# Optimization experiments

Hardware: AMD Instinct MI355X
Metric: run time of the kernel (lower is better)

## Reference

```python
import jax, jax.numpy as jnp
import numpy as np

N_TRAIN = 131072
M_TEST = 65536
T_SPAN = 100.0
D = 3  # Matern-5/2 state dim


def setup_inputs() -> dict:
    key = jax.random.key(0)
    k1, k2, k3, k4 = jax.random.split(key, 4)
    times = jnp.sort(jax.random.uniform(k1, (N_TRAIN,), jnp.float32) * T_SPAN)
    t_star = jnp.sort(jax.random.uniform(k2, (M_TEST,), jnp.float32) * T_SPAN)
    # positive site precisions, site naturals scaled so pseudo-targets are O(1)
    site_nat2 = jax.random.uniform(k3, (N_TRAIN,), jnp.float32) * 4.0 + 0.5
    site_nat1 = jax.random.normal(k4, (N_TRAIN,), jnp.float32) * site_nat2
    return dict(
        times=times,
        t_star=t_star,
        site_nat1=site_nat1,
        site_nat2=site_nat2,
        variance=jnp.float32(1.0),
        lengthscale=jnp.float32(0.5),
        mean_const=jnp.float32(0.1),
    )


def _matern52_sde(variance, lengthscale):
    lam = jnp.sqrt(5.0).astype(jnp.float32) / lengthscale
    F = jnp.array([[0.0, 1.0, 0.0],
                   [0.0, 0.0, 1.0],
                   [0.0, 0.0, 0.0]], jnp.float32)
    F = F.at[2, 0].set(-lam ** 3).at[2, 1].set(-3.0 * lam ** 2).at[2, 2].set(-3.0 * lam)
    kappa = lam ** 2 / 3.0
    P_inf = variance * jnp.array([[1.0, 0.0, 0.0],
                                  [0.0, 0.0, 0.0],
                                  [0.0, 0.0, 0.0]], jnp.float32)
    P_inf = P_inf.at[0, 2].set(-variance * kappa)
    P_inf = P_inf.at[2, 0].set(-variance * kappa)
    P_inf = P_inf.at[1, 1].set(variance * kappa)
    P_inf = P_inf.at[2, 2].set(variance * lam ** 4)
    H = jnp.array([[1.0, 0.0, 0.0]], jnp.float32)
    return F, H, P_inf, lam


def _discretise(F, P_inf, lam, dt):
    # (F + lam I) is nilpotent of index 3 -> exact expm
    I = jnp.eye(D, dtype=jnp.float32)
    Nm = F + lam * I
    Nm2 = Nm @ Nm
    dt_ = dt[:, None, None]
    A = jnp.exp(-lam * dt)[:, None, None] * (I + dt_ * Nm + 0.5 * dt_ ** 2 * Nm2)
    APA = jnp.einsum('tij,jk,tlk->til', A, P_inf, A)
    Q = P_inf - APA
    return A, Q


def _kalman_filter(H, P_inf, A_seq, Q_seq, residual, is_obs, R_full):
    h = H[0]  # [D]

    def step(carry, inp):
        m, P = carry
        A, Q, r, obs, R = inp
        m_pred = A @ m
        P_pred = A @ P @ A.T + Q
        S = h @ P_pred @ h + R
        K = obs * (P_pred @ h) / S  # masked gain: test points skip update
        v = r - m_pred @ h
        m_f = m_pred + K * v
        P_f = P_pred - jnp.outer(K, K) * S
        return (m_f, P_f), (m_pred, P_pred, m_f, P_f)

    init = (jnp.zeros(D, jnp.float32), P_inf)
    _, (m_pred, P_pred, m_filt, P_filt) = jax.lax.scan(
        step, init, (A_seq, Q_seq, residual, is_obs, R_full))
    return m_pred, P_pred, m_filt, P_filt


def _rts_smoother(m_pred, P_pred, m_filt, P_filt, A_seq):
    def back(carry, inp):
        m_s_next, P_s_next = carry
        m_f, P_f, A_n, m_p_n, P_p_n = inp
        G = jnp.linalg.solve(P_p_n, A_n @ P_f).T  # P_f A^T P_pred^{-1}
        m_s = m_f + G @ (m_s_next - m_p_n)
        P_s = P_f + G @ (P_s_next - P_p_n) @ G.T
        return (m_s, P_s), (m_s, P_s)

    init = (m_filt[-1], P_filt[-1])
    xs = (m_filt[:-1], P_filt[:-1], A_seq[1:], m_pred[1:], P_pred[1:])
    _, (m_s, P_s) = jax.lax.scan(back, init, xs, reverse=True)
    m_smooth = jnp.concatenate([m_s, m_filt[-1:]], axis=0)
    P_smooth = jnp.concatenate([P_s, P_filt[-1:]], axis=0)
    return m_smooth, P_smooth


def reference(times, t_star, site_nat1, site_nat2, variance, lengthscale, mean_const):
    F, H, P_inf, lam = _matern52_sde(variance, lengthscale)
    N = times.shape[0]
    M = t_star.shape[0]
    merged = jnp.concatenate([times, t_star])
    order = jnp.argsort(merged)  # jnp.argsort is stable
    merged_sorted = merged[order]
    is_obs = jnp.concatenate([jnp.ones(N, jnp.float32), jnp.zeros(M, jnp.float32)])[order]
    pseudo_targets = site_nat1 / site_nat2
    residual_full = jnp.concatenate([pseudo_targets - mean_const,
                                     jnp.zeros(M, jnp.float32)])[order]
    R_full = jnp.concatenate([jnp.reciprocal(site_nat2), jnp.ones(M, jnp.float32)])[order]
    dt_full = jnp.concatenate([jnp.zeros(1, jnp.float32), jnp.diff(merged_sorted)])
    A_seq, Q_seq = _discretise(F, P_inf, lam, dt_full)
    m_pred, P_pred, m_filt, P_filt = _kalman_filter(
        H, P_inf, A_seq, Q_seq, residual_full, is_obs, R_full)
    m_smooth, P_smooth = _rts_smoother(m_pred, P_pred, m_filt, P_filt, A_seq)
    inv_order = jnp.argsort(order)
    test_positions = inv_order[N:]
    m_test = m_smooth[test_positions]
    P_test = P_smooth[test_positions]
    means = m_test @ H[0] + mean_const  # H = [1,0,0]
    vars_ = jnp.einsum('i,tij,j->t', H[0], P_test, H[0])
    return means, jnp.maximum(vars_, 0.0)
```

## Files before the change

### kernel.cpp

```cpp
#include <hip/hip_runtime.h>
#include <math.h>

#define DEV __device__ __forceinline__

constexpr int N_TRAIN = 131072;
constexpr int M_TEST  = 65536;
constexpr int T_TOT   = N_TRAIN + M_TEST;
constexpr int TPB     = 64;
constexpr int NBLK    = T_TOT / TPB;
constexpr int GRP     = 64;
constexpr int NGRP    = NBLK / GRP;
constexpr int FE_S    = 33;
constexpr int SE_S    = 19;

DEV void mm(const float* X, const float* Y, float* Z) {
#pragma unroll
  for (int i = 0; i < 3; ++i)
#pragma unroll
    for (int j = 0; j < 3; ++j)
      Z[i*3+j] = X[i*3]*Y[j] + X[i*3+1]*Y[3+j] + X[i*3+2]*Y[6+j];
}
DEV void mmnt(const float* X, const float* Y, float* Z) {
#pragma unroll
  for (int i = 0; i < 3; ++i)
#pragma unroll
    for (int j = 0; j < 3; ++j)
      Z[i*3+j] = X[i*3]*Y[j*3] + X[i*3+1]*Y[j*3+1] + X[i*3+2]*Y[j*3+2];
}
DEV void mtn(const float* X, const float* Y, float* Z) {
#pragma unroll
  for (int i = 0; i < 3; ++i)
#pragma unroll
    for (int j = 0; j < 3; ++j)
      Z[i*3+j] = X[i]*Y[j] + X[3+i]*Y[3+j] + X[6+i]*Y[6+j];
}
DEV void mv(const float* X, const float* v, float* w) {
#pragma unroll
  for (int i = 0; i < 3; ++i) w[i] = X[i*3]*v[0] + X[i*3+1]*v[1] + X[i*3+2]*v[2];
}
DEV void mtv(const float* X, const float* v, float* w) {
#pragma unroll
  for (int i = 0; i < 3; ++i) w[i] = X[i]*v[0] + X[3+i]*v[1] + X[6+i]*v[2];
}
DEV void inv3(const float* mf_, float* o) {
  double m0=mf_[0], m1=mf_[1], m2=mf_[2], m3=mf_[3], m4=mf_[4],
         m5=mf_[5], m6=mf_[6], m7=mf_[7], m8=mf_[8];
  double c00 = m4*m8 - m5*m7;
  double c10 = m5*m6 - m3*m8;
  double c20 = m3*m7 - m4*m6;
  double det = m0*c00 + m1*c10 + m2*c20;
  double id = 1.0 / det;
  o[0] = (float)(c00*id); o[1] = (float)((m2*m7-m1*m8)*id); o[2] = (float)((m1*m5-m2*m4)*id);
  o[3] = (float)(c10*id); o[4] = (float)((m0*m8-m2*m6)*id); o[5] = (float)((m2*m3-m0*m5)*id);
  o[6] = (float)(c20*id); o[7] = (float)((m1*m6-m0*m7)*id); o[8] = (float)((m0*m4-m1*m3)*id);
}
DEV void symm(float* P) {
  float a = 0.5f*(P[1]+P[3]), b = 0.5f*(P[2]+P[6]), c = 0.5f*(P[5]+P[7]);
  P[1]=P[3]=a; P[2]=P[6]=b; P[5]=P[7]=c;
}

struct Model { float lam, v, kap, l4; };
DEV Model make_model(const float* varp, const float* ellp) {
  Model M; M.v = varp[0];
  float ell = ellp[0];
  M.lam = sqrtf(5.0f) / ell;
  M.kap = M.lam * M.lam / 3.0f;
  float l2 = M.lam * M.lam;
  M.l4 = l2 * l2;
  return M;
}
DEV void pinf(const Model& M, float* P) {
  float vk = M.v * M.kap;
  P[0]=M.v; P[1]=0;  P[2]=-vk;
  P[3]=0;   P[4]=vk; P[5]=0;
  P[6]=-vk; P[7]=0;  P[8]=M.v*M.l4;
}
DEV void make_AQ(const Model& M, float dt, float* A, float* Q) {
  float lam = M.lam, l2 = lam*lam, l3 = l2*lam, l4 = M.l4;
  float e = __expf(-lam * dt);
  float h = 0.5f * dt * dt;
  A[0] = e*(1.0f + dt*lam + h*l2);
  A[1] = e*(dt + 2.0f*h*lam);
  A[2] = e*h;
  A[3] = e*(-h*l3);
  A[4] = e*(1.0f + dt*lam - 2.0f*h*l2);
  A[5] = e*(dt - h*lam);
  A[6] = e*(-dt*l3 + h*l4);
  A[7] = e*(-3.0f*dt*l2 + 2.0f*h*l3);
  A[8] = e*(1.0f - 2.0f*dt*lam + h*l2);
  float vk = M.v * M.kap, vl4 = M.v * M.l4;
  float B[9];
#pragma unroll
  for (int i = 0; i < 3; ++i) {
    B[i*3+0] =  A[i*3+0]*M.v - A[i*3+2]*vk;
    B[i*3+1] =  A[i*3+1]*vk;
    B[i*3+2] = -A[i*3+0]*vk  + A[i*3+2]*vl4;
  }
  float Pi[9]; pinf(M, Pi);
#pragma unroll
  for (int i = 0; i < 3; ++i)
#pragma unroll
    for (int j = 0; j < 3; ++j)
      Q[i*3+j] = Pi[i*3+j] - (B[i*3]*A[j*3] + B[i*3+1]*A[j*3+1] + B[i*3+2]*A[j*3+2]);
}

struct FE { float A[9]; float b[3]; float C[9]; float h[3]; float J[9]; };

DEV FE fe_identity() {
  FE e;
#pragma unroll
  for (int i=0;i<9;++i){ e.A[i]=0.0f; e.C[i]=0.0f; e.J[i]=0.0f; }
  e.A[0]=e.A[4]=e.A[8]=1.0f;
  e.b[0]=e.b[1]=e.b[2]=0.0f; e.h[0]=e.h[1]=e.h[2]=0.0f;
  return e;
}
DEV void fe_store(const FE& e, float* g) {
#pragma unroll
  for (int i=0;i<9;++i) g[i]=e.A[i];
  g[9]=e.b[0]; g[10]=e.b[1]; g[11]=e.b[2];
#pragma unroll
  for (int i=0;i<9;++i) g[12+i]=e.C[i];
  g[21]=e.h[0]; g[22]=e.h[1]; g[23]=e.h[2];
#pragma unroll
  for (int i=0;i<9;++i) g[24+i]=e.J[i];
}
DEV FE fe_load(const float* g) {
  FE e;
#pragma unroll
  for (int i=0;i<9;++i) e.A[i]=g[i];
  e.b[0]=g[9]; e.b[1]=g[10]; e.b[2]=g[11];
#pragma unroll
  for (int i=0;i<9;++i) e.C[i]=g[12+i];
  e.h[0]=g[21]; e.h[1]=g[22]; e.h[2]=g[23];
#pragma unroll
  for (int i=0;i<9;++i) e.J[i]=g[24+i];
  return e;
}
DEV void fe_storeT(const FE& e, float* g, int idx, int n) {
#pragma unroll
  for (int i=0;i<9;++i) g[i*n+idx]=e.A[i];
#pragma unroll
  for (int i=0;i<3;++i) g[(9+i)*n+idx]=e.b[i];
#pragma unroll
  for (int i=0;i<9;++i) g[(12+i)*n+idx]=e.C[i];
#pragma unroll
  for (int i=0;i<3;++i) g[(21+i)*n+idx]=e.h[i];
#pragma unroll
  for (int i=0;i<9;++i) g[(24+i)*n+idx]=e.J[i];
}
DEV FE fe_loadT(const float* g, int idx, int n) {
  FE e;
#pragma unroll
  for (int i=0;i<9;++i) e.A[i]=g[i*n+idx];
#pragma unroll
  for (int i=0;i<3;++i) e.b[i]=g[(9+i)*n+idx];
#pragma unroll
  for (int i=0;i<9;++i) e.C[i]=g[(12+i)*n+idx];
#pragma unroll
  for (int i=0;i<3;++i) e.h[i]=g[(21+i)*n+idx];
#pragma unroll
  for (int i=0;i<9;++i) e.J[i]=g[(24+i)*n+idx];
  return e;
}
DEV FE build_felem(const Model& M, float dt, float obsf, float rf, float Rf_, bool first) {
  FE E;
  float r = rf, R = Rf_;
  float g = (obsf > 0.5f) ? 1.0f : 0.0f;
  if (first) {
#pragma unroll
    for (int i=0;i<9;++i){ E.A[i]=0.0f; E.J[i]=0.0f; }
    E.h[0]=E.h[1]=E.h[2]=0.0f;
    float Pi[9]; pinf(M, Pi);
    float S = Pi[0] + R;
    float f = g / S;
    float K0=Pi[0]*f, K1=Pi[3]*f, K2=Pi[6]*f;
    E.b[0]=K0*r; E.b[1]=K1*r; E.b[2]=K2*r;
    E.C[0]=Pi[0]-S*K0*K0; E.C[1]=Pi[1]-S*K0*K1; E.C[2]=Pi[2]-S*K0*K2;
    E.C[3]=Pi[3]-S*K1*K0; E.C[4]=Pi[4]-S*K1*K1; E.C[5]=Pi[5]-S*K1*K2;
    E.C[6]=Pi[6]-S*K2*K0; E.C[7]=Pi[7]-S*K2*K1; E.C[8]=Pi[8]-S*K2*K2;
    return E;
  }
  float Am[9], Q[9]; make_AQ(M, dt, Am, Q);
  float S = Q[0] + R, iS = g / S;
  float K0=Q[0]*iS, K1=Q[3]*iS, K2=Q[6]*iS;
#pragma unroll
  for (int j = 0; j < 3; ++j) {
    E.A[j]   = Am[j]   - K0*Am[j];
    E.A[3+j] = Am[3+j] - K1*Am[j];
    E.A[6+j] = Am[6+j] - K2*Am[j];
    E.C[j]   = Q[j]    - K0*Q[j];
    E.C[3+j] = Q[3+j]  - K1*Q[j];
    E.C[6+j] = Q[6+j]  - K2*Q[j];
  }
  E.b[0]=K0*r; E.b[1]=K1*r; E.b[2]=K2*r;
  float riS = r*iS;
  E.h[0]=Am[0]*riS; E.h[1]=Am[1]*riS; E.h[2]=Am[2]*riS;
#pragma unroll
  for (int i = 0; i < 3; ++i)
#pragma unroll
    for (int j = 0; j < 3; ++j)
      E.J[i*3+j] = Am[i]*Am[j]*iS;
  return E;
}
DEV FE fcompose(const FE& x, const FE& y) {
  const float *A1=x.A,*b1=x.b,*C1=x.C,*h1=x.h,*J1=x.J;
  const float *A2=y.A,*b2=y.b,*C2=y.C,*h2=y.h,*J2=y.J;
  FE o;
  float Mx[9]; mm(C1,J2,Mx); Mx[0]+=1.0f; Mx[4]+=1.0f; Mx[8]+=1.0f;
  float Mi[9]; inv3(Mx,Mi);
  float T1[9]; mm(A2,Mi,T1);
  mm(T1,A1,o.A);
  float u[3]; mv(C1,h2,u); u[0]+=b1[0]; u[1]+=b1[1]; u[2]+=b1[2];
  mv(T1,u,o.b); o.b[0]+=b2[0]; o.b[1]+=b2[1]; o.b[2]+=b2[2];
  float t2[9]; mm(T1,C1,t2);
  mmnt(t2,A2,o.C);
#pragma unroll
  for (int i=0;i<9;++i) o.C[i]+=C2[i];
  float tmp[9]; mm(Mi,A1,tmp);
  float w[3]; mv(J2,b1,w);
  w[0]=h2[0]-w[0]; w[1]=h2[1]-w[1]; w[2]=h2[2]-w[2];
  mtv(tmp,w,o.h); o.h[0]+=h1[0]; o.h[1]+=h1[1]; o.h[2]+=h1[2];
  float V[9]; mm(J2,A1,V);
  mtn(tmp,V,o.J);
#pragma unroll
  for (int i=0;i<9;++i) o.J[i]+=J1[i];
  symm(o.C); symm(o.J);
  return o;
}
DEV void fstep(const Model& M, float dt, float obsf, float rf, float Rf_,
               float* m, float* P) {
  float A[9], Q[9]; make_AQ(M, dt, A, Q);
  float mp[3]; mv(A, m, mp);
  float W[9]; mmnt(P, A, W);
  float Pp[9]; mm(A, W, Pp);
#pragma unroll
  for (int i=0;i<9;++i) Pp[i]+=Q[i];
  float S = Pp[0] + Rf_;
  float f = (obsf > 0.5f) ? (1.0f/S) : 0.0f;
  float K0=Pp[0]*f, K1=Pp[3]*f, K2=Pp[6]*f;
  float v = rf - mp[0];
  m[0]=mp[0]+K0*v; m[1]=mp[1]+K1*v; m[2]=mp[2]+K2*v;
  P[0]=Pp[0]-S*K0*K0; P[1]=Pp[1]-S*K0*K1; P[2]=Pp[2]-S*K0*K2;
  P[3]=Pp[3]-S*K1*K0; P[4]=Pp[4]-S*K1*K1; P[5]=Pp[5]-S*K1*K2;
  P[6]=Pp[6]-S*K2*K0; P[7]=Pp[7]-S*K2*K1; P[8]=Pp[8]-S*K2*K2;
  symm(P);
}

struct SE { float G[9]; float c[3]; float U[9]; };

DEV SE se_identity() {
  SE s;
#pragma unroll
  for (int i=0;i<9;++i){ s.G[i]=0.0f; s.U[i]=0.0f; }
  s.G[0]=s.G[4]=s.G[8]=1.0f;
  s.c[0]=s.c[1]=s.c[2]=0.0f;
  return s;
}
DEV void se_store(const SE& s, float* g) {
#pragma unroll
  for (int i=0;i<9;++i) g[i]=s.G[i];
  g[9]=s.c[0]; g[10]=s.c[1]; g[11]=s.c[2];
  g[12]=s.U[0]; g[13]=s.U[1]; g[14]=s.U[2]; g[15]=s.U[4]; g[16]=s.U[5]; g[17]=s.U[8];
}
DEV SE se_load(const float* g) {
  SE s;
#pragma unroll
  for (int i=0;i<9;++i) s.G[i]=g[i];
  s.c[0]=g[9]; s.c[1]=g[10]; s.c[2]=g[11];
  s.U[0]=g[12]; s.U[1]=g[13]; s.U[2]=g[14];
  s.U[3]=g[13]; s.U[4]=g[15]; s.U[5]=g[16];
  s.U[6]=g[14]; s.U[7]=g[16]; s.U[8]=g[17];
  return s;
}
DEV void se_storeT(const SE& s, float* g, int idx, int n) {
#pragma unroll
  for (int i=0;i<9;++i) g[i*n+idx]=s.G[i];
#pragma unroll
  for (int i=0;i<3;++i) g[(9+i)*n+idx]=s.c[i];
  g[12*n+idx]=s.U[0]; g[13*n+idx]=s.U[1]; g[14*n+idx]=s.U[2];
  g[15*n+idx]=s.U[4]; g[16*n+idx]=s.U[5]; g[17*n+idx]=s.U[8];
}
DEV SE se_loadT(const float* g, int idx, int n) {
  SE s;
#pragma unroll
  for (int i=0;i<9;++i) s.G[i]=g[i*n+idx];
#pragma unroll
  for (int i=0;i<3;++i) s.c[i]=g[(9+i)*n+idx];
  float u0=g[12*n+idx], u1=g[13*n+idx], u2=g[14*n+idx],
        u4=g[15*n+idx], u5=g[16*n+idx], u8=g[17*n+idx];
  s.U[0]=u0; s.U[1]=u1; s.U[2]=u2;
  s.U[3]=u1; s.U[4]=u4; s.U[5]=u5;
  s.U[6]=u2; s.U[7]=u5; s.U[8]=u8;
  return s;
}
DEV SE scompose(const SE& x, const SE& y) {
  SE o;
  mm(x.G, y.G, o.G);
  float t[3]; mv(x.G, y.c, t);
  o.c[0]=t[0]+x.c[0]; o.c[1]=t[1]+x.c[1]; o.c[2]=t[2]+x.c[2];
  float T[9]; mm(x.G, y.U, T);
  mmnt(T, x.G, o.U);
#pragma unroll
  for (int i=0;i<9;++i) o.U[i]+=x.U[i];
  symm(o.U);
  return o;
}
DEV void sapply(const SE& s, float* m, float* P) {
  float t[3]; mv(s.G, m, t);
  float T[9]; mm(s.G, P, T);
  float Pn[9]; mmnt(T, s.G, Pn);
  m[0]=t[0]+s.c[0]; m[1]=t[1]+s.c[1]; m[2]=t[2]+s.c[2];
#pragma unroll
  for (int i=0;i<9;++i) P[i]=Pn[i]+s.U[i];
  symm(P);
}
DEV SE build_selem(const Model& M, const float4* pk, const float* mf, const float* Pf, int k) {
  float m[3] = { mf[k], mf[T_TOT+k], mf[2*T_TOT+k] };
  float p00=Pf[k], p01=Pf[T_TOT+k], p02=Pf[2*T_TOT+k],
        p11=Pf[3*T_TOT+k], p12=Pf[4*T_TOT+k], p22=Pf[5*T_TOT+k];
  float P[9] = { p00,p01,p02, p01,p11,p12, p02,p12,p22 };
  float dt = pk[k+1].x - pk[k].x;
  SE s;
  float A[9], Q[9]; make_AQ(M, dt, A, Q);
  float W[9]; mmnt(P, A, W);
  float Pp[9]; mm(A, W, Pp);
#pragma unroll
  for (int j=0;j<9;++j) Pp[j]+=Q[j];
  float Pi_[9]; inv3(Pp, Pi_);
  mm(W, Pi_, s.G);
  float mp[3]; mv(A, m, mp);
  float gm[3]; mv(s.G, mp, gm);
  s.c[0]=m[0]-gm[0]; s.c[1]=m[1]-gm[1]; s.c[2]=m[2]-gm[2];
  float GW[9]; mmnt(s.G, W, GW);
#pragma unroll
  for (int j=0;j<9;++j) s.U[j]=P[j]-GW[j];
  symm(s.U);
  return s;
}

__global__ void k_merge(const float* __restrict__ times, const float* __restrict__ tstar,
                        const float* __restrict__ n1, const float* __restrict__ n2,
                        const float* __restrict__ mcp,
                        float4* pk, int* oix) {
  int g = blockIdx.x*blockDim.x + threadIdx.x;
  if (g >= T_TOT) return;
  float mc = mcp[0];
  if (g < N_TRAIN) {
    int i = g;
    float t = times[i];
    int lo = 0, hi = M_TEST;
    while (lo < hi) { int mid=(lo+hi)>>1; if (tstar[mid] < t) lo=mid+1; else hi=mid; }
    int p = i + lo;
    float s2 = n2[i];
    pk[p] = make_float4(t, n1[i]/s2 - mc, 1.0f/s2, 1.0f);
    oix[p] = -1;
  } else {
    int j = g - N_TRAIN;
    float t = tstar[j];
    int lo = 0, hi = N_TRAIN;
    while (lo < hi) { int mid=(lo+hi)>>1; if (times[mid] <= t) lo=mid+1; else hi=mid; }
    int p = j + lo;
    pk[p] = make_float4(t, 0.f, 1.f, 0.f);
    oix[p] = j;
  }
}

__global__ __launch_bounds__(TPB, 2) void k_f1(
    const float* varp, const float* ellp, const float4* __restrict__ pk,
    float* tIncl, float* blkAgg) {
  __shared__ float lds[TPB*FE_S];
  int l = threadIdx.x, b = blockIdx.x;
  int t = b*TPB + l;
  Model M = make_model(varp, ellp);
  float4 q = pk[t];
  float dt = (t == 0) ? 0.0f : (q.x - pk[t-1].x);
  FE run = build_felem(M, dt, q.w, q.y, q.z, t == 0);
  fe_store(run, &lds[l*FE_S]);
  for (int d = 1; d < TPB; d <<= 1) {
    __syncthreads();
    FE oth; bool act = (l >= d);
    if (act) oth = fe_load(&lds[(l-d)*FE_S]);
    __syncthreads();
    if (act) { run = fcompose(oth, run); fe_store(run, &lds[l*FE_S]); }
  }
  fe_storeT(run, tIncl, t, T_TOT);
  if (l == TPB-1) fe_storeT(run, blkAgg, b, NBLK);
}

__global__ __launch_bounds__(TPB, 2) void k_f2a(const float* __restrict__ blkAgg,
                                                float* blkIncl2, float* grpAgg) {
  __shared__ float lds[TPB*FE_S];
  int l = threadIdx.x, gb = blockIdx.x;
  int b = gb*GRP + l;
  FE run = fe_loadT(blkAgg, b, NBLK);
  fe_store(run, &lds[l*FE_S]);
  for (int d = 1; d < TPB; d <<= 1) {
    __syncthreads();
    FE oth; bool act = (l >= d);
    if (act) oth = fe_load(&lds[(l-d)*FE_S]);
    __syncthreads();
    if (act) { run = fcompose(oth, run); fe_store(run, &lds[l*FE_S]); }
  }
  fe_storeT(run, blkIncl2, b, NBLK);
  if (l == GRP-1) fe_store(run, grpAgg + gb*FE_S);
}

__global__ __launch_bounds__(TPB, 2) void k_f2b(const float* __restrict__ grpAgg,
                                                float* grpPref) {
  __shared__ float lds[TPB*FE_S];
  int j = threadIdx.x;
  FE run = (j < NGRP) ? fe_load(grpAgg + j*FE_S) : fe_identity();
  fe_store(run, &lds[j*FE_S]);
  for (int d = 1; d < TPB; d <<= 1) {
    __syncthreads();
    FE oth; bool act = (j >= d);
    if (act) oth = fe_load(&lds[(j-d)*FE_S]);
    __syncthreads();
    if (act) { run = fcompose(oth, run); fe_store(run, &lds[j*FE_S]); }
  }
  __syncthreads();
  if (j < NGRP) {
    FE X = (j == 0) ? fe_identity() : fe_load(&lds[(j-1)*FE_S]);
    fe_store(X, grpPref + j*FE_S);
  }
}

__global__ __launch_bounds__(TPB, 2) void k_f3(
    const float* varp, const float* ellp, const float4* __restrict__ pk,
    const float* __restrict__ tIncl, const float* __restrict__ blkIncl2,
    const float* __restrict__ grpPref,
    float* mf, float* Pf, float* xT) {
  int l = threadIdx.x, b = blockIdx.x;
  int t = b*TPB + l;
  int g = b >> 6, lb = b & (GRP-1);
  Model M = make_model(varp, ellp);
  float m[3], P[9];
  if (t == 0) {
    m[0]=m[1]=m[2]=0.0f; pinf(M, P);
  } else {
    FE gp = fe_load(grpPref + g*FE_S);
    FE entB = (lb == 0) ? gp : fcompose(gp, fe_loadT(blkIncl2, b-1, NBLK));
    FE ent  = (l == 0) ? entB : fcompose(entB, fe_loadT(tIncl, t-1, T_TOT));
    m[0]=ent.b[0]; m[1]=ent.b[1]; m[2]=ent.b[2];
#pragma unroll
    for (int i=0;i<9;++i) P[i]=ent.C[i];
  }
  float4 q = pk[t];
  float dt = (t == 0) ? 0.0f : (q.x - pk[t-1].x);
  fstep(M, dt, q.w, q.y, q.z, m, P);
  mf[t]=m[0]; mf[T_TOT+t]=m[1]; mf[2*T_TOT+t]=m[2];
  Pf[t]=P[0]; Pf[T_TOT+t]=P[1]; Pf[2*T_TOT+t]=P[2];
  Pf[3*T_TOT+t]=P[4]; Pf[4*T_TOT+t]=P[5]; Pf[5*T_TOT+t]=P[8];
  if (t == T_TOT-1) {
    xT[0]=m[0]; xT[1]=m[1]; xT[2]=m[2];
    xT[3]=P[0]; xT[4]=P[1]; xT[5]=P[2];
    xT[6]=P[4]; xT[7]=P[5]; xT[8]=P[8];
  }
}

__global__ __launch_bounds__(TPB, 2) void k_s1(
    const float* varp, const float* ellp, const float4* __restrict__ pk,
    const float* __restrict__ mf, const float* __restrict__ Pf,
    float* tSuf, float* blkAggS) {
  __shared__ float lds[TPB*SE_S];
  int l = threadIdx.x, b = blockIdx.x;
  int t = b*TPB + l;
  Model M = make_model(varp, ellp);
  SE Macc = (t <= T_TOT-2) ? build_selem(M, pk, mf, Pf, t) : se_identity();
  se_store(Macc, &lds[l*SE_S]);
  for (int d = 1; d < TPB; d <<= 1) {
    __syncthreads();
    SE oth; bool act = (l + d < TPB);
    if (act) oth = se_load(&lds[(l+d)*SE_S]);
    __syncthreads();
    if (act) { Macc = scompose(Macc, oth); se_store(Macc, &lds[l*SE_S]); }
  }
  se_storeT(Macc, tSuf, t, T_TOT);
  if (l == 0) se_storeT(Macc, blkAggS, b, NBLK);
}

__global__ __launch_bounds__(TPB, 2) void k_s2a(const float* __restrict__ blkAggS,
                                                float* blkSuf2, float* grpAggS) {
  __shared__ float lds[TPB*SE_S];
  int l = threadIdx.x, gb = blockIdx.x;
  int b = gb*GRP + l;
  SE run = se_loadT(blkAggS, b, NBLK);
  se_store(run, &lds[l*SE_S]);
  for (int d = 1; d < TPB; d <<= 1) {
    __syncthreads();
    SE oth; bool act = (l + d < TPB);
    if (act) oth = se_load(&lds[(l+d)*SE_S]);
    __syncthreads();
    if (act) { run = scompose(run, oth); se_store(run, &lds[l*SE_S]); }
  }
  se_storeT(run, blkSuf2, b, NBLK);
  if (l == 0) se_store(run, grpAggS + gb*18);
}

__global__ __launch_bounds__(TPB, 2) void k_s2b(const float* __restrict__ grpAggS,
                                                const float* __restrict__ xT,
                                                float* gExit) {
  __shared__ float lds[TPB*SE_S];
  int j = threadIdx.x;
  SE run = (j < NGRP) ? se_load(grpAggS + j*18) : se_identity();
  se_store(run, &lds[j*SE_S]);
  for (int d = 1; d < TPB; d <<= 1) {
    __syncthreads();
    SE oth; bool act = (j + d < TPB);
    if (act) oth = se_load(&lds[(j+d)*SE_S]);
    __syncthreads();
    if (act) { run = scompose(run, oth); se_store(run, &lds[j*SE_S]); }
  }
  __syncthreads();
  if (j < NGRP) {
    float m[3] = { xT[0], xT[1], xT[2] };
    float P[9] = { xT[3],xT[4],xT[5], xT[4],xT[6],xT[7], xT[5],xT[7],xT[8] };
    if (j < NGRP-1) {
      SE Sx = se_load(&lds[(j+1)*SE_S]);
      sapply(Sx, m, P);
    }
    float* o = gExit + j*9;
    o[0]=m[0];o[1]=m[1];o[2]=m[2];o[3]=P[0];o[4]=P[1];o[5]=P[2];o[6]=P[4];o[7]=P[5];o[8]=P[8];
  }
}

__global__ __launch_bounds__(TPB, 2) void k_s3(
    const float* varp, const float* ellp, const float* mcp,
    const float4* __restrict__ pk,
    const float* __restrict__ mf, const float* __restrict__ Pf,
    const float* __restrict__ tSuf, const float* __restrict__ blkSuf2,
    const float* __restrict__ gExit,
    const int* __restrict__ oix, float* out) {
  int l = threadIdx.x, b = blockIdx.x;
  int t = b*TPB + l;
  int g = b >> 6, lb = b & (GRP-1);
  Model M = make_model(varp, ellp);
  float mc = mcp[0];
  const float* ge = gExit + g*9;
  float m[3] = { ge[0], ge[1], ge[2] };
  float P[9] = { ge[3],ge[4],ge[5], ge[4],ge[6],ge[7], ge[5],ge[7],ge[8] };
  if (lb < GRP-1) {
    SE s = se_loadT(blkSuf2, b+1, NBLK);
    sapply(s, m, P);
  }
  if (l < TPB-1) {
    SE s = se_loadT(tSuf, t+1, T_TOT);
    sapply(s, m, P);
  }
  if (t <= T_TOT-2) {
    SE e = build_selem(M, pk, mf, Pf, t);
    sapply(e, m, P);
  }
  int j = oix[t];
  if (j >= 0) { out[j] = m[0] + mc; out[M_TEST + j] = fmaxf(P[0], 0.0f); }
}

extern "C" void kernel_launch(void* const* d_in, const int* in_sizes, int n_in,
                              void* d_out, int out_size, void* d_ws, size_t ws_size,
                              hipStream_t stream) {
  const float* times = (const float*)d_in[0];
  const float* tstar = (const float*)d_in[1];
  const float* n1    = (const float*)d_in[2];
  const float* n2    = (const float*)d_in[3];
  const float* varp  = (const float*)d_in[4];
  const float* ellp  = (const float*)d_in[5];
  const float* mcp   = (const float*)d_in[6];
  float* out = (float*)d_out;

  size_t off = 0;
  auto take = [&](size_t bytes) {
    char* p = (char*)d_ws + off;
    off += (bytes + 255) & ~(size_t)255;
    return (void*)p;
  };
  float4* pk     = (float4*)take(sizeof(float4) * T_TOT);
  int*    oix    = (int*)   take(sizeof(int)    * T_TOT);
  float*  mf     = (float*) take(sizeof(float)  * 3 * T_TOT);
  float*  Pf     = (float*) take(sizeof(float)  * 6 * T_TOT);
  float*  tIncl  = (float*) take(sizeof(float)  * FE_S * T_TOT);
  float*  blkAgg = (float*) take(sizeof(float)  * FE_S * NBLK);
  float*  blkIncl2=(float*) take(sizeof(float)  * FE_S * NBLK);
  float*  grpAgg = (float*) take(sizeof(float)  * FE_S * NGRP);
  float*  grpPref= (float*) take(sizeof(float)  * FE_S * NGRP);
  float*  tSuf   = (float*) take(sizeof(float)  * 18 * T_TOT);
  float*  blkAggS= (float*) take(sizeof(float)  * 18 * NBLK);
  float*  blkSuf2= (float*) take(sizeof(float)  * 18 * NBLK);
  float*  grpAggS= (float*) take(sizeof(float)  * 18 * NGRP);
  float*  gExit  = (float*) take(sizeof(float)  * 9  * NGRP);
  float*  xT     = (float*) take(sizeof(float)  * 9);
  (void)ws_size; (void)in_sizes; (void)n_in; (void)out_size;

  k_merge<<<(T_TOT+255)/256, 256, 0, stream>>>(times, tstar, n1, n2, mcp, pk, oix);
  k_f1   <<<NBLK, TPB, 0, stream>>>(varp, ellp, pk, tIncl, blkAgg);
  k_f2a  <<<NGRP, TPB, 0, stream>>>(blkAgg, blkIncl2, grpAgg);
  k_f2b  <<<1, TPB, 0, stream>>>(grpAgg, grpPref);
  k_f3   <<<NBLK, TPB, 0, stream>>>(varp, ellp, pk, tIncl, blkIncl2, grpPref, mf, Pf, xT);
  k_s1   <<<NBLK, TPB, 0, stream>>>(varp, ellp, pk, mf, Pf, tSuf, blkAggS);
  k_s2a  <<<NGRP, TPB, 0, stream>>>(blkAggS, blkSuf2, grpAggS);
  k_s2b  <<<1, TPB, 0, stream>>>(grpAggS, xT, gExit);
  k_s3   <<<NBLK, TPB, 0, stream>>>(varp, ellp, mcp, pk, mf, Pf, tSuf, blkSuf2, gExit, oix, out);
}
```

Before: 157.1 us.

## Replace LDS scans with wavefront shuffles and cache smoother elements

Each 64-thread block is a single wavefront, so the Hillis-Steele scans in all six scan kernels now exchange elements with __shfl_up/__shfl_down instead of going through shared memory with two barriers per step. k_s1 also stores each smoother element to a new eSel buffer, so k_s3 loads it rather than rebuilding it from pk/mf/Pf. Some launch bounds are raised to allow more resident blocks. The trade-off is extra global traffic for eSel and compose work now done by every lane, including inactive ones; the identity element for the last smoother step must match the earlier skip.

```diff
diff --git a/kernel.cpp b/kernel.cpp
--- a/kernel.cpp
+++ b/kernel.cpp
@@ -11,7 +11,6 @@
 constexpr int GRP     = 64;
 constexpr int NGRP    = NBLK / GRP;
 constexpr int FE_S    = 33;
-constexpr int SE_S    = 19;
 
 DEV void mm(const float* X, const float* Y, float* Z) {
 #pragma unroll
@@ -162,6 +161,20 @@
   for (int i=0;i<9;++i) e.J[i]=g[(24+i)*n+idx];
   return e;
 }
+DEV FE fe_shfl_up(const FE& e, int d) {
+  FE o;
+#pragma unroll
+  for (int i=0;i<9;++i) o.A[i]=__shfl_up(e.A[i], d, 64);
+#pragma unroll
+  for (int i=0;i<3;++i) o.b[i]=__shfl_up(e.b[i], d, 64);
+#pragma unroll
+  for (int i=0;i<9;++i) o.C[i]=__shfl_up(e.C[i], d, 64);
+#pragma unroll
+  for (int i=0;i<3;++i) o.h[i]=__shfl_up(e.h[i], d, 64);
+#pragma unroll
+  for (int i=0;i<9;++i) o.J[i]=__shfl_up(e.J[i], d, 64);
+  return o;
+}
 DEV FE build_felem(const Model& M, float dt, float obsf, float rf, float Rf_, bool first) {
   FE E;
   float r = rf, R = Rf_;
@@ -292,6 +305,16 @@
   s.U[3]=u1; s.U[4]=u4; s.U[5]=u5;
   s.U[6]=u2; s.U[7]=u5; s.U[8]=u8;
   return s;
+}
+DEV SE se_shfl_down(const SE& s, int d) {
+  SE o;
+#pragma unroll
+  for (int i=0;i<9;++i) o.G[i]=__shfl_down(s.G[i], d, 64);
+#pragma unroll
+  for (int i=0;i<3;++i) o.c[i]=__shfl_down(s.c[i], d, 64);
+#pragma unroll
+  for (int i=0;i<9;++i) o.U[i]=__shfl_down(s.U[i], d, 64);
+  return o;
 }
 DEV SE scompose(const SE& x, const SE& y) {
   SE o;
@@ -365,23 +388,19 @@
   }
 }
 
-__global__ __launch_bounds__(TPB, 2) void k_f1(
+__global__ __launch_bounds__(TPB, 3) void k_f1(
     const float* varp, const float* ellp, const float4* __restrict__ pk,
     float* tIncl, float* blkAgg) {
-  __shared__ float lds[TPB*FE_S];
   int l = threadIdx.x, b = blockIdx.x;
   int t = b*TPB + l;
   Model M = make_model(varp, ellp);
   float4 q = pk[t];
   float dt = (t == 0) ? 0.0f : (q.x - pk[t-1].x);
   FE run = build_felem(M, dt, q.w, q.y, q.z, t == 0);
-  fe_store(run, &lds[l*FE_S]);
   for (int d = 1; d < TPB; d <<= 1) {
-    __syncthreads();
-    FE oth; bool act = (l >= d);
-    if (act) oth = fe_load(&lds[(l-d)*FE_S]);
-    __syncthreads();
-    if (act) { run = fcompose(oth, run); fe_store(run, &lds[l*FE_S]); }
+    FE oth = fe_shfl_up(run, d);
+    FE comp = fcompose(oth, run);
+    if (l >= d) run = comp;
   }
   fe_storeT(run, tIncl, t, T_TOT);
   if (l == TPB-1) fe_storeT(run, blkAgg, b, NBLK);
@@ -389,17 +408,13 @@
 
 __global__ __launch_bounds__(TPB, 2) void k_f2a(const float* __restrict__ blkAgg,
                                                 float* blkIncl2, float* grpAgg) {
-  __shared__ float lds[TPB*FE_S];
   int l = threadIdx.x, gb = blockIdx.x;
   int b = gb*GRP + l;
   FE run = fe_loadT(blkAgg, b, NBLK);
-  fe_store(run, &lds[l*FE_S]);
   for (int d = 1; d < TPB; d <<= 1) {
-    __syncthreads();
-    FE oth; bool act = (l >= d);
-    if (act) oth = fe_load(&lds[(l-d)*FE_S]);
-    __syncthreads();
-    if (act) { run = fcompose(oth, run); fe_store(run, &lds[l*FE_S]); }
+    FE oth = fe_shfl_up(run, d);
+    FE comp = fcompose(oth, run);
+    if (l >= d) run = comp;
   }
   fe_storeT(run, blkIncl2, b, NBLK);
   if (l == GRP-1) fe_store(run, grpAgg + gb*FE_S);
@@ -407,25 +422,21 @@
 
 __global__ __launch_bounds__(TPB, 2) void k_f2b(const float* __restrict__ grpAgg,
                                                 float* grpPref) {
-  __shared__ float lds[TPB*FE_S];
   int j = threadIdx.x;
   FE run = (j < NGRP) ? fe_load(grpAgg + j*FE_S) : fe_identity();
-  fe_store(run, &lds[j*FE_S]);
   for (int d = 1; d < TPB; d <<= 1) {
-    __syncthreads();
-    FE oth; bool act = (j >= d);
-    if (act) oth = fe_load(&lds[(j-d)*FE_S]);
-    __syncthreads();
-    if (act) { run = fcompose(oth, run); fe_store(run, &lds[j*FE_S]); }
-  }
-  __syncthreads();
+    FE oth = fe_shfl_up(run, d);
+    FE comp = fcompose(oth, run);
+    if (j >= d) run = comp;
+  }
+  FE X = fe_shfl_up(run, 1);
   if (j < NGRP) {
-    FE X = (j == 0) ? fe_identity() : fe_load(&lds[(j-1)*FE_S]);
+    if (j == 0) X = fe_identity();
     fe_store(X, grpPref + j*FE_S);
   }
 }
 
-__global__ __launch_bounds__(TPB, 2) void k_f3(
+__global__ __launch_bounds__(TPB, 3) void k_f3(
     const float* varp, const float* ellp, const float4* __restrict__ pk,
     const float* __restrict__ tIncl, const float* __restrict__ blkIncl2,
     const float* __restrict__ grpPref,
@@ -458,22 +469,20 @@
   }
 }
 
-__global__ __launch_bounds__(TPB, 2) void k_s1(
+__global__ __launch_bounds__(TPB, 3) void k_s1(
     const float* varp, const float* ellp, const float4* __restrict__ pk,
     const float* __restrict__ mf, const float* __restrict__ Pf,
-    float* tSuf, float* blkAggS) {
-  __shared__ float lds[TPB*SE_S];
+    float* eSel, float* tSuf, float* blkAggS) {
   int l = threadIdx.x, b = blockIdx.x;
   int t = b*TPB + l;
   Model M = make_model(varp, ellp);
-  SE Macc = (t <= T_TOT-2) ? build_selem(M, pk, mf, Pf, t) : se_identity();
-  se_store(Macc, &lds[l*SE_S]);
+  SE e = (t <= T_TOT-2) ? build_selem(M, pk, mf, Pf, t) : se_identity();
+  se_storeT(e, eSel, t, T_TOT);
+  SE Macc = e;
   for (int d = 1; d < TPB; d <<= 1) {
-    __syncthreads();
-    SE oth; bool act = (l + d < TPB);
-    if (act) oth = se_load(&lds[(l+d)*SE_S]);
-    __syncthreads();
-    if (act) { Macc = scompose(Macc, oth); se_store(Macc, &lds[l*SE_S]); }
+    SE oth = se_shfl_down(Macc, d);
+    SE comp = scompose(Macc, oth);
+    if (l + d < TPB) Macc = comp;
   }
   se_storeT(Macc, tSuf, t, T_TOT);
   if (l == 0) se_storeT(Macc, blkAggS, b, NBLK);
@@ -481,17 +490,13 @@
 
 __global__ __launch_bounds__(TPB, 2) void k_s2a(const float* __restrict__ blkAggS,
                                                 float* blkSuf2, float* grpAggS) {
-  __shared__ float lds[TPB*SE_S];
   int l = threadIdx.x, gb = blockIdx.x;
   int b = gb*GRP + l;
   SE run = se_loadT(blkAggS, b, NBLK);
-  se_store(run, &lds[l*SE_S]);
   for (int d = 1; d < TPB; d <<= 1) {
-    __syncthreads();
-    SE oth; bool act = (l + d < TPB);
-    if (act) oth = se_load(&lds[(l+d)*SE_S]);
-    __syncthreads();
-    if (act) { run = scompose(run, oth); se_store(run, &lds[l*SE_S]); }
+    SE oth = se_shfl_down(run, d);
+    SE comp = scompose(run, oth);
+    if (l + d < TPB) run = comp;
   }
   se_storeT(run, blkSuf2, b, NBLK);
   if (l == 0) se_store(run, grpAggS + gb*18);
@@ -500,41 +505,31 @@
 __global__ __launch_bounds__(TPB, 2) void k_s2b(const float* __restrict__ grpAggS,
                                                 const float* __restrict__ xT,
                                                 float* gExit) {
-  __shared__ float lds[TPB*SE_S];
   int j = threadIdx.x;
   SE run = (j < NGRP) ? se_load(grpAggS + j*18) : se_identity();
-  se_store(run, &lds[j*SE_S]);
   for (int d = 1; d < TPB; d <<= 1) {
-    __syncthreads();
-    SE oth; bool act = (j + d < TPB);
-    if (act) oth = se_load(&lds[(j+d)*SE_S]);
-    __syncthreads();
-    if (act) { run = scompose(run, oth); se_store(run, &lds[j*SE_S]); }
-  }
-  __syncthreads();
+    SE oth = se_shfl_down(run, d);
+    SE comp = scompose(run, oth);
+    if (j + d < TPB) run = comp;
+  }
+  SE Sx = se_shfl_down(run, 1);
   if (j < NGRP) {
     float m[3] = { xT[0], xT[1], xT[2] };
     float P[9] = { xT[3],xT[4],xT[5], xT[4],xT[6],xT[7], xT[5],xT[7],xT[8] };
-    if (j < NGRP-1) {
-      SE Sx = se_load(&lds[(j+1)*SE_S]);
-      sapply(Sx, m, P);
-    }
+    if (j < NGRP-1) sapply(Sx, m, P);
     float* o = gExit + j*9;
     o[0]=m[0];o[1]=m[1];o[2]=m[2];o[3]=P[0];o[4]=P[1];o[5]=P[2];o[6]=P[4];o[7]=P[5];o[8]=P[8];
   }
 }
 
-__global__ __launch_bounds__(TPB, 2) void k_s3(
-    const float* varp, const float* ellp, const float* mcp,
-    const float4* __restrict__ pk,
-    const float* __restrict__ mf, const float* __restrict__ Pf,
-    const float* __restrict__ tSuf, const float* __restrict__ blkSuf2,
-    const float* __restrict__ gExit,
+__global__ __launch_bounds__(TPB, 4) void k_s3(
+    const float* mcp,
+    const float* __restrict__ eSel, const float* __restrict__ tSuf,
+    const float* __restrict__ blkSuf2, const float* __restrict__ gExit,
     const int* __restrict__ oix, float* out) {
   int l = threadIdx.x, b = blockIdx.x;
   int t = b*TPB + l;
   int g = b >> 6, lb = b & (GRP-1);
-  Model M = make_model(varp, ellp);
   float mc = mcp[0];
   const float* ge = gExit + g*9;
   float m[3] = { ge[0], ge[1], ge[2] };
@@ -547,8 +542,8 @@
     SE s = se_loadT(tSuf, t+1, T_TOT);
     sapply(s, m, P);
   }
-  if (t <= T_TOT-2) {
-    SE e = build_selem(M, pk, mf, Pf, t);
+  {
+    SE e = se_loadT(eSel, t, T_TOT);
     sapply(e, m, P);
   }
   int j = oix[t];
@@ -582,6 +577,7 @@
   float*  blkIncl2=(float*) take(sizeof(float)  * FE_S * NBLK);
   float*  grpAgg = (float*) take(sizeof(float)  * FE_S * NGRP);
   float*  grpPref= (float*) take(sizeof(float)  * FE_S * NGRP);
+  float*  eSel   = (float*) take(sizeof(float)  * 18 * T_TOT);
   float*  tSuf   = (float*) take(sizeof(float)  * 18 * T_TOT);
   float*  blkAggS= (float*) take(sizeof(float)  * 18 * NBLK);
   float*  blkSuf2= (float*) take(sizeof(float)  * 18 * NBLK);
@@ -595,8 +591,8 @@
   k_f2a  <<<NGRP, TPB, 0, stream>>>(blkAgg, blkIncl2, grpAgg);
   k_f2b  <<<1, TPB, 0, stream>>>(grpAgg, grpPref);
   k_f3   <<<NBLK, TPB, 0, stream>>>(varp, ellp, pk, tIncl, blkIncl2, grpPref, mf, Pf, xT);
-  k_s1   <<<NBLK, TPB, 0, stream>>>(varp, ellp, pk, mf, Pf, tSuf, blkAggS);
+  k_s1   <<<NBLK, TPB, 0, stream>>>(varp, ellp, pk, mf, Pf, eSel, tSuf, blkAggS);
   k_s2a  <<<NGRP, TPB, 0, stream>>>(blkAggS, blkSuf2, grpAggS);
   k_s2b  <<<1, TPB, 0, stream>>>(grpAggS, xT, gExit);
-  k_s3   <<<NBLK, TPB, 0, stream>>>(varp, ellp, mcp, pk, mf, Pf, tSuf, blkSuf2, gExit, oix, out);
-}
+  k_s3   <<<NBLK, TPB, 0, stream>>>(mcp, eSel, tSuf, blkSuf2, gExit, oix, out);
+}
```

Measured after the change: 150.5 us. 1.04x faster.
